# Kernel optimization log

Measured on AMD Instinct MI355X. Metric: run time of the kernel, lower is better.

The kernel has to match this reference:

```python
import jax, jax.numpy as jnp
import numpy as np

E, C, F, K = 8, 768, 3072, 2  # NUM_EXPERTS, EMBED_DIM, FFN_DIM, TOP_K


def setup_inputs() -> dict:
    key = jax.random.key(0)
    k0, k1, k2, k3 = jax.random.split(key, 4)
    B, T = 8, 2048
    return {
        "x": jax.random.normal(k0, (B, T, C), jnp.float32),
        "router_w": jax.random.normal(k1, (E, C), jnp.float32) * 0.02,
        "w1": jax.random.normal(k2, (E, C, F), jnp.float32) * 0.02,
        "b1": jnp.zeros((E, F), jnp.float32),
        "w2": jax.random.normal(k3, (E, F, C), jnp.float32) * 0.02,
        "b2": jnp.zeros((E, C), jnp.float32),
    }


def reference(x, router_w, w1, b1, w2, b2):
    # Dropout is inference-mode identity (eval). GELU is torch's exact (erf) variant.
    B, T, Cc = x.shape
    flat = x.reshape(-1, Cc)                                   # [N, C]
    logits = flat @ router_w.T                                 # [N, E]
    probs = jax.nn.softmax(logits.astype(jnp.float32), axis=-1)
    top_w, top_i = jax.lax.top_k(probs, K)                     # [N, K]
    top_w = (top_w / top_w.sum(-1, keepdims=True)).astype(x.dtype)
    out = jnp.zeros_like(flat)
    for e in range(E):
        # per-token combine weight for expert e (0 if token not routed to e)
        w_e = jnp.sum(top_w * (top_i == e), axis=-1)[:, None]  # [N, 1]
        h = jax.nn.gelu(flat @ w1[e] + b1[e], approximate=False)  # [N, F]
        out = out + w_e * (h @ w2[e] + b2[e])
    return out.reshape(B, T, Cc)
```

## Files before the change

### kernel.cpp

```cpp
#include <hip/hip_runtime.h>
#include <hip/hip_bf16.h>

#define NTOK 16384
#define CDIM 768
#define FDIM 3072
#define NEXP 8
#define NSLOT 32768
#define HBLK 128
#define MAXTILES 263

typedef __attribute__((ext_vector_type(8))) short bf16x8;
typedef __attribute__((ext_vector_type(4))) float f32x4;
typedef __attribute__((ext_vector_type(8))) unsigned short u16x8;

__device__ __forceinline__ unsigned short f2bf(float f) {
  unsigned int u = __float_as_uint(f);
  u += 0x7FFFu + ((u >> 16) & 1u);
  return (unsigned short)(u >> 16);
}
__device__ __forceinline__ float bf2f(unsigned short h) {
  return __uint_as_float((unsigned int)h << 16);
}

__device__ __forceinline__ float fast_gelu(float x) {
  float x2 = x * x;
  float z = x * __builtin_fmaf(0.070565402f, x2, 1.5975981f);
  float s = __builtin_amdgcn_rcpf(1.0f + __expf(-z));
  return x * s;
}

__device__ __forceinline__ void async16(const void* g, void* l) {
  __builtin_amdgcn_global_load_lds(
      (const __attribute__((address_space(1))) unsigned int*)g,
      (__attribute__((address_space(3))) unsigned int*)l, 16, 0, 0);
}

__global__ __launch_bounds__(256)
void k_transpose(const float* __restrict__ src, unsigned short* __restrict__ dst,
                 int R, int Cc)
{
  __shared__ float tle[32][33];
  int e = blockIdx.z;
  int c0 = blockIdx.x * 32, r0 = blockIdx.y * 32;
  int tx = threadIdx.x & 31, ty = threadIdx.x >> 5;
  const float* s = src + (size_t)e * R * Cc;
  unsigned short* d = dst + (size_t)e * R * Cc;
#pragma unroll
  for (int i = 0; i < 4; ++i)
    tle[ty + i * 8][tx] = s[(size_t)(r0 + ty + i * 8) * Cc + c0 + tx];
  __syncthreads();
#pragma unroll
  for (int i = 0; i < 4; ++i)
    d[(size_t)(c0 + ty + i * 8) * R + r0 + tx] = f2bf(tle[tx][ty + i * 8]);
}

__global__ __launch_bounds__(256)
void k_router(const float* __restrict__ x, const float* __restrict__ rw,
              int* __restrict__ tk_e, float* __restrict__ tk_w)
{
  __shared__ float srw[NEXP * CDIM];
  int tid = threadIdx.x;
#pragma unroll
  for (int i = 0; i < (NEXP * CDIM / 4) / 256; ++i)
    ((float4*)srw)[tid + i * 256] = ((const float4*)rw)[tid + i * 256];
  __syncthreads();
  int lane = tid & 63, wid = tid >> 6;
  int t = blockIdx.x * 4 + wid;
  float a[NEXP];
#pragma unroll
  for (int e = 0; e < NEXP; ++e) a[e] = 0.f;
  const float* xr = x + (size_t)t * CDIM;
#pragma unroll
  for (int c = 0; c < CDIM / 64; ++c) {
    float xv = xr[c * 64 + lane];
#pragma unroll
    for (int e = 0; e < NEXP; ++e) a[e] += xv * srw[e * CDIM + c * 64 + lane];
  }
#pragma unroll
  for (int e = 0; e < NEXP; ++e) {
#pragma unroll
    for (int off = 32; off; off >>= 1) a[e] += __shfl_xor(a[e], off);
  }
  if (lane == 0) {
    int i0 = 0; float l0 = a[0];
#pragma unroll
    for (int e = 1; e < NEXP; ++e) if (a[e] > l0) { l0 = a[e]; i0 = e; }
    int i1 = -1; float l1 = -1e30f;
#pragma unroll
    for (int e = 0; e < NEXP; ++e) if (e != i0 && a[e] > l1) { l1 = a[e]; i1 = e; }
    float w0 = 1.f / (1.f + expf(l1 - l0));
    tk_e[2 * t] = i0;     tk_e[2 * t + 1] = i1;
    tk_w[2 * t] = w0;     tk_w[2 * t + 1] = 1.f - w0;
  }
}

__global__ __launch_bounds__(256)
void k_hist(const int* __restrict__ tk_e, int* __restrict__ blockhist)
{
  __shared__ int h[NEXP];
  int tid = threadIdx.x;
  if (tid < NEXP) h[tid] = 0;
  __syncthreads();
  int e = tk_e[blockIdx.x * 256 + tid];
  atomicAdd(&h[e], 1);
  __syncthreads();
  if (tid < NEXP) blockhist[blockIdx.x * NEXP + tid] = h[tid];
}

__global__ __launch_bounds__(512)
void k_scan2(const int* __restrict__ blockhist, int* __restrict__ counts,
             int* __restrict__ offsets, int* __restrict__ tp,
             int* __restrict__ blockbase)
{
  __shared__ int ltot[NEXP];
  __shared__ int loff[NEXP + 1];
  int tid = threadIdx.x;
  int lane = tid & 63, e = tid >> 6;
  int o0 = blockhist[lane * NEXP + e];
  int o1 = blockhist[(64 + lane) * NEXP + e];
  int h0 = o0, h1 = o1;
#pragma unroll
  for (int d = 1; d < 64; d <<= 1) { int v = __shfl_up(h0, d); if (lane >= d) h0 += v; }
  int s0 = __shfl(h0, 63);
#pragma unroll
  for (int d = 1; d < 64; d <<= 1) { int v = __shfl_up(h1, d); if (lane >= d) h1 += v; }
  h1 += s0;
  if (lane == 63) ltot[e] = h1;
  __syncthreads();
  if (tid == 0) {
    loff[0] = 0;
    int tpv = 0; tp[0] = 0;
    for (int k = 0; k < NEXP; ++k) {
      loff[k + 1] = loff[k] + ltot[k];
      counts[k] = ltot[k];
      offsets[k] = loff[k];
      tpv += (ltot[k] + 127) / 128;
      tp[k + 1] = tpv;
    }
    offsets[NEXP] = loff[NEXP];
  }
  __syncthreads();
  int base = loff[e];
  blockbase[lane * NEXP + e]        = base + h0 - o0;
  blockbase[(64 + lane) * NEXP + e] = base + h1 - o1;
}

__global__ __launch_bounds__(256)
void k_assign_gather(const float* __restrict__ x, const int* __restrict__ tk_e,
                     const float* __restrict__ tk_w,
                     const int* __restrict__ blockbase,
                     int* __restrict__ tok2slot, float* __restrict__ slot_w,
                     unsigned short* __restrict__ Xg)
{
  __shared__ int eh[256];
  __shared__ int sslot[256];
  int b = blockIdx.x, tid = threadIdx.x;
  int pick = b * 256 + tid;
  int e = tk_e[pick];
  eh[tid] = e;
  __syncthreads();
  int rank = 0;
  for (int j = 0; j < tid; ++j) rank += (eh[j] == e);
  int slot = blockbase[b * NEXP + e] + rank;
  sslot[tid] = slot;
  tok2slot[pick] = slot;
  slot_w[slot] = tk_w[pick];
  __syncthreads();
  int lane = tid & 63, wid = tid >> 6;
  for (int p = wid * 64; p < wid * 64 + 64; ++p) {
    int token = (b * 256 + p) >> 1;
    int s = sslot[p];
    const float4* src = (const float4*)(x + (size_t)token * CDIM);
    ushort4* dst = (ushort4*)(Xg + (size_t)s * CDIM);
#pragma unroll
    for (int i = 0; i < 3; ++i) {
      float4 v = src[i * 64 + lane];
      ushort4 hh;
      hh.x = f2bf(v.x); hh.y = f2bf(v.y); hh.z = f2bf(v.z); hh.w = f2bf(v.w);
      dst[i * 64 + lane] = hh;
    }
  }
}

__global__ __launch_bounds__(512, 4)
void k_gemm1(const unsigned short* __restrict__ A, int lda,
             const unsigned short* __restrict__ B, int ldb, long sB,
             int Ksteps, const int* __restrict__ counts,
             const int* __restrict__ offsets, const int* __restrict__ tp,
             int t0, const float* __restrict__ bias, int biasStride,
             unsigned short* __restrict__ Hout, int ldh, int gx, int nwg)
{
  __shared__ __align__(16) char lds[3 * 24576];

  int orig = blockIdx.y * gx + blockIdx.x;
  int q = nwg >> 3, r = nwg & 7;
  int xcd = orig & 7, jj = orig >> 3;
  int wgid = (xcd < r ? xcd * (q + 1) : r * (q + 1) + (xcd - r) * q) + jj;
  const int RG = 16;
  int yT = nwg / gx;
  int gsize = gx * RG;
  int rg = wgid / gsize;
  int rem = wgid - rg * gsize;
  int rgs = yT - rg * RG; if (rgs > RG) rgs = RG;
  int bx = rem / rgs;
  int byl = rg * RG + (rem - bx * rgs);
  int by = t0 + byl;

  if (by >= tp[NEXP]) return;
  int e = 0;
  while (by >= tp[e + 1]) ++e;
  int m0 = (by - tp[e]) * 128;
  int cnt = counts[e];
  int rowbase = offsets[e];
  int n0 = bx * 256;

  const unsigned short* Bexp = B + (long)e * sB + (long)n0 * ldb;
  const unsigned short* Aexp = A + (long)(rowbase + m0) * lda;

  int tid = threadIdx.x;
  int lane = tid & 63, wid = tid >> 6;
  int wm = wid >> 2, wn = wid & 3;
  int ar = lane & 15, kg = lane >> 4;
  int kgs = (kg ^ ((ar >> 1) & 3)) << 4;

  int rA0 = tid >> 2;
  int cA0 = tid & 3;
  int ksw = (cA0 ^ ((rA0 >> 1) & 3)) << 3;
  const unsigned short* As0 = Aexp + (long)rA0 * lda + ksw;
  const unsigned short* Bs0 = Bexp + (long)rA0 * ldb + ksw;
  const unsigned short* Bs1 = Bexp + (long)(rA0 + 128) * ldb + ksw;

  f32x4 acc[4][4] = {};

  auto STAGE = [&](int buf, int t) {
    char* bb = lds + buf * 24576;
    int ko = t * 32;
    async16(As0 + ko, bb + wid * 1024);
    async16(Bs0 + ko, bb + 8192 + wid * 1024);
    async16(Bs1 + ko, bb + 16384 + wid * 1024);
  };

  STAGE(0, 0); STAGE(1, 1);
  int cur = 0, nxt2 = 2;

  for (int ks = 0; ks < Ksteps; ++ks) {
    if (ks + 1 < Ksteps) {
      asm volatile("s_waitcnt vmcnt(3)" ::: "memory");
    } else {
      asm volatile("s_waitcnt vmcnt(0)" ::: "memory");
    }
    __builtin_amdgcn_s_barrier();
    asm volatile("" ::: "memory");

    const char* bb = lds + cur * 24576;
    const char* bA = bb + (wm * 64 + ar) * 64 + kgs;
    const char* bB = bb + 8192 + (wn * 64 + ar) * 64 + kgs;
    bf16x8 af[4], bfr[4];
#pragma unroll
    for (int i = 0; i < 4; ++i) af[i] = *(const bf16x8*)(bA + i * 1024);
#pragma unroll
    for (int i = 0; i < 4; ++i) bfr[i] = *(const bf16x8*)(bB + i * 1024);

    if (ks + 2 < Ksteps) STAGE(nxt2, ks + 2);

#pragma unroll
    for (int mi = 0; mi < 4; ++mi)
#pragma unroll
      for (int ni = 0; ni < 4; ++ni)
        acc[mi][ni] = __builtin_amdgcn_mfma_f32_16x16x32_bf16(af[mi], bfr[ni],
                                                              acc[mi][ni], 0, 0, 0);
    cur = (cur == 2) ? 0 : cur + 1;
    nxt2 = (nxt2 == 2) ? 0 : nxt2 + 1;
  }

  unsigned short* st = (unsigned short*)lds;
  __syncthreads();

#pragma unroll
  for (int ni = 0; ni < 4; ++ni) {
    int col = wn * 64 + ni * 16 + ar;
    float bv = bias[e * biasStride + n0 + col];
#pragma unroll
    for (int mi = 0; mi < 4; ++mi) {
#pragma unroll
      for (int rr = 0; rr < 4; ++rr) {
        int row = wm * 64 + mi * 16 + kg * 4 + rr;
        float v = fast_gelu(acc[mi][ni][rr] + bv);
        st[row * 264 + col] = f2bf(v);
      }
    }
  }
  __syncthreads();
  int row = tid >> 2, qq = tid & 3;
  unsigned short* drow = Hout + (long)(byl * 128 + row) * ldh + n0 + qq * 64;
  const unsigned short* srow = st + row * 264 + qq * 64;
#pragma unroll
  for (int i = 0; i < 8; ++i)
    *(u16x8*)(drow + i * 8) = *(const u16x8*)(srow + i * 8);
}

__global__ __launch_bounds__(256, 3)
void k_gemm2(const unsigned short* __restrict__ A, int lda,
             const unsigned short* __restrict__ B, int ldb, long sB,
             int Ksteps, const int* __restrict__ counts,
             const int* __restrict__ offsets, const int* __restrict__ tp,
             int t0, const float* __restrict__ bias, int biasStride,
             unsigned short* __restrict__ Yout, const float* __restrict__ slot_w,
             int gx, int nwg)
{
  __shared__ __align__(16) char lds[3 * 16384];

  int orig = blockIdx.y * gx + blockIdx.x;
  int q = nwg >> 3, r = nwg & 7;
  int xcd = orig & 7, jj = orig >> 3;
  int wgid = (xcd < r ? xcd * (q + 1) : r * (q + 1) + (xcd - r) * q) + jj;
  const int RG = 16;
  int yT = nwg / gx;
  int gsize = gx * RG;
  int rg = wgid / gsize;
  int rem = wgid - rg * gsize;
  int rgs = yT - rg * RG; if (rgs > RG) rgs = RG;
  int bx = rem / rgs;
  int byl = rg * RG + (rem - bx * rgs);
  int by = t0 + byl;

  if (by >= tp[NEXP]) return;
  int e = 0;
  while (by >= tp[e + 1]) ++e;
  int m0 = (by - tp[e]) * 128;
  int cnt = counts[e];
  int rowbase = offsets[e];
  int n0 = bx * 128;

  const unsigned short* Bexp = B + (long)e * sB + (long)n0 * ldb;
  const unsigned short* Aexp = A + (long)(byl * 128) * lda;

  int tid = threadIdx.x;
  int lane = tid & 63, wid = tid >> 6;
  int wm = wid >> 1, wn = wid & 1;
  int ar = lane & 15, kg = lane >> 4;
  int kgs = (kg ^ ((ar >> 1) & 3)) << 4;

  int rA0 = tid >> 2;
  int cA0 = tid & 3;
  int ksw = (cA0 ^ ((rA0 >> 1) & 3)) << 3;
  const unsigned short* As0 = Aexp + (long)rA0 * lda + ksw;
  const unsigned short* As1 = Aexp + (long)(rA0 + 64) * lda + ksw;
  const unsigned short* Bs0 = Bexp + (long)rA0 * ldb + ksw;
  const unsigned short* Bs1 = Bexp + (long)(rA0 + 64) * ldb + ksw;

  f32x4 acc[4][4] = {};

  auto STAGE = [&](int buf, int t) {
    char* bb = lds + buf * 16384;
    int ko = t * 32;
    async16(As0 + ko, bb + wid * 1024);
    async16(As1 + ko, bb + 4096 + wid * 1024);
    async16(Bs0 + ko, bb + 8192 + wid * 1024);
    async16(Bs1 + ko, bb + 12288 + wid * 1024);
  };

  STAGE(0, 0); STAGE(1, 1);
  int cur = 0, nxt2 = 2;

  for (int ks = 0; ks < Ksteps; ++ks) {
    if (ks + 1 < Ksteps) {
      asm volatile("s_waitcnt vmcnt(4)" ::: "memory");
    } else {
      asm volatile("s_waitcnt vmcnt(0)" ::: "memory");
    }
    __builtin_amdgcn_s_barrier();
    asm volatile("" ::: "memory");

    const char* bb = lds + cur * 16384;
    const char* bA = bb + (wm * 64 + ar) * 64 + kgs;
    const char* bB = bb + 8192 + (wn * 64 + ar) * 64 + kgs;
    bf16x8 af[4], bfr[4];
#pragma unroll
    for (int i = 0; i < 4; ++i) af[i] = *(const bf16x8*)(bA + i * 1024);
#pragma unroll
    for (int i = 0; i < 4; ++i) bfr[i] = *(const bf16x8*)(bB + i * 1024);

    if (ks + 2 < Ksteps) STAGE(nxt2, ks + 2);

#pragma unroll
    for (int mi = 0; mi < 4; ++mi)
#pragma unroll
      for (int ni = 0; ni < 4; ++ni)
        acc[mi][ni] = __builtin_amdgcn_mfma_f32_16x16x32_bf16(af[mi], bfr[ni],
                                                              acc[mi][ni], 0, 0, 0);
    cur = (cur == 2) ? 0 : cur + 1;
    nxt2 = (nxt2 == 2) ? 0 : nxt2 + 1;
  }

  unsigned short* st = (unsigned short*)lds;
  __syncthreads();

#pragma unroll
  for (int mi = 0; mi < 4; ++mi) {
#pragma unroll
    for (int rr = 0; rr < 4; ++rr) {
      int rowl = wm * 64 + mi * 16 + kg * 4 + rr;
      float wt = (m0 + rowl < cnt) ? slot_w[rowbase + m0 + rowl] : 0.f;
#pragma unroll
      for (int ni = 0; ni < 4; ++ni) {
        int col = wn * 64 + ni * 16 + ar;
        float v = (acc[mi][ni][rr] + bias[e * biasStride + n0 + col]) * wt;
        st[rowl * 136 + col] = f2bf(v);
      }
    }
  }
  __syncthreads();
  int row = tid >> 1, half = tid & 1;
  if (m0 + row < cnt) {
    unsigned short* drow = Yout + (long)(rowbase + m0 + row) * CDIM + n0 + half * 64;
    const unsigned short* srow = st + row * 136 + half * 64;
#pragma unroll
    for (int i = 0; i < 8; ++i)
      *(u16x8*)(drow + i * 8) = *(const u16x8*)(srow + i * 8);
  }
}

__global__ __launch_bounds__(256)
void k_combine(const unsigned short* __restrict__ Y,
               const int* __restrict__ tok2slot, float* __restrict__ out)
{
  int t = blockIdx.x * 4 + (threadIdx.x >> 6);
  int lane = threadIdx.x & 63;
  int s0 = tok2slot[2 * t], s1 = tok2slot[2 * t + 1];
  const ushort4* y0 = (const ushort4*)(Y + (size_t)s0 * CDIM);
  const ushort4* y1 = (const ushort4*)(Y + (size_t)s1 * CDIM);
  float4* o = (float4*)(out + (size_t)t * CDIM);
#pragma unroll
  for (int i = 0; i < 3; ++i) {
    ushort4 a = y0[i * 64 + lane];
    ushort4 b = y1[i * 64 + lane];
    float4 r;
    r.x = bf2f(a.x) + bf2f(b.x);
    r.y = bf2f(a.y) + bf2f(b.y);
    r.z = bf2f(a.z) + bf2f(b.z);
    r.w = bf2f(a.w) + bf2f(b.w);
    o[i * 64 + lane] = r;
  }
}

extern "C" void kernel_launch(void* const* d_in, const int* in_sizes, int n_in,
                              void* d_out, int out_size, void* d_ws, size_t ws_size,
                              hipStream_t stream) {
  const float* x        = (const float*)d_in[0];
  const float* router_w = (const float*)d_in[1];
  const float* w1       = (const float*)d_in[2];
  const float* b1       = (const float*)d_in[3];
  const float* w2       = (const float*)d_in[4];
  const float* b2       = (const float*)d_in[5];
  float* out = (float*)d_out;

  char* ws = (char*)d_ws;
  size_t off = 0;
  auto alloc = [&](size_t bytes) -> void* {
    void* p = ws + off;
    off = (off + bytes + 255) & ~(size_t)255;
    return p;
  };
  int*   counts     = (int*)alloc(NEXP * 4);
  int*   offsets    = (int*)alloc((NEXP + 1) * 4);
  int*   tp         = (int*)alloc((NEXP + 1) * 4);
  int*   tk_e       = (int*)alloc((size_t)NSLOT * 4);
  float* tk_w       = (float*)alloc((size_t)NSLOT * 4);
  int*   blockhist  = (int*)alloc((size_t)HBLK * NEXP * 4);
  int*   blockbase  = (int*)alloc((size_t)HBLK * NEXP * 4);
  int*   tok2slot   = (int*)alloc((size_t)NSLOT * 4);
  float* slot_w     = (float*)alloc((size_t)NSLOT * 4);
  unsigned short* Yslot = (unsigned short*)alloc((size_t)NSLOT * CDIM * 2);
  unsigned short* w1t = (unsigned short*)alloc((size_t)NEXP * FDIM * CDIM * 2);
  unsigned short* w2t = (unsigned short*)alloc((size_t)NEXP * CDIM * FDIM * 2);
  unsigned short* Xg  = (unsigned short*)alloc((size_t)(NSLOT + 256) * CDIM * 2);
  int TPC = 66;
  if (off + ((size_t)TPC * 128 + 128) * FDIM * 2 > ws_size) TPC = 33;
  unsigned short* H = (unsigned short*)alloc(((size_t)TPC * 128 + 128) * FDIM * 2);

  k_transpose<<<dim3(FDIM / 32, CDIM / 32, NEXP), 256, 0, stream>>>(w1, w1t, CDIM, FDIM);
  k_transpose<<<dim3(CDIM / 32, FDIM / 32, NEXP), 256, 0, stream>>>(w2, w2t, FDIM, CDIM);
  k_router<<<NTOK / 4, 256, 0, stream>>>(x, router_w, tk_e, tk_w);
  k_hist<<<HBLK, 256, 0, stream>>>(tk_e, blockhist);
  k_scan2<<<1, 512, 0, stream>>>(blockhist, counts, offsets, tp, blockbase);
  k_assign_gather<<<HBLK, 256, 0, stream>>>(x, tk_e, tk_w, blockbase,
                                            tok2slot, slot_w, Xg);

  for (int t0 = 0; t0 < MAXTILES; t0 += TPC) {
    int yT = (MAXTILES - t0 < TPC) ? (MAXTILES - t0) : TPC;
    int gx1 = FDIM / 256;
    k_gemm1<<<dim3(gx1, yT), 512, 0, stream>>>(
        Xg, CDIM, w1t, CDIM, (long)FDIM * CDIM, CDIM / 32,
        counts, offsets, tp, t0, b1, FDIM, H, FDIM, gx1, gx1 * yT);
    int gx2 = CDIM / 128;
    k_gemm2<<<dim3(gx2, yT), 256, 0, stream>>>(
        H, FDIM, w2t, FDIM, (long)CDIM * FDIM, FDIM / 32,
        counts, offsets, tp, t0, b2, CDIM, Yslot, slot_w, gx2, gx2 * yT);
  }
  k_combine<<<NTOK / 4, 256, 0, stream>>>(Yslot, tok2slot, out);
}
```

Baseline: 665.6 us.

## Use 256x256 tiles in gemm1 with 8-phase ping-pong LDS pipeline

Expert GEMM1 now computes 256-row by 256-column tiles per workgroup instead of 128x256. It uses 128 KB of double-buffered LDS with K=64 stages, an XOR swizzle, and eight barrier-separated MFMA phases per iteration, with s_setprio raised around the MFMA blocks. Expert tile padding moves to 256 rows and gemm2 is remapped to two 128-row halves per 256-row tile, skipping empty halves. This is meant to raise arithmetic intensity and overlap loads with MFMA. In exchange it cuts occupancy to 2 waves per SIMD, increases padding waste per expert, and adds many barriers.

```diff
diff --git a/kernel.cpp b/kernel.cpp
--- a/kernel.cpp
+++ b/kernel.cpp
@@ -7,7 +7,7 @@
 #define NEXP 8
 #define NSLOT 32768
 #define HBLK 128
-#define MAXTILES 263
+#define MAXT256 135
 
 typedef __attribute__((ext_vector_type(8))) short bf16x8;
 typedef __attribute__((ext_vector_type(4))) float f32x4;
@@ -34,6 +34,10 @@
       (const __attribute__((address_space(1))) unsigned int*)g,
       (__attribute__((address_space(3))) unsigned int*)l, 16, 0, 0);
 }
+
+#define BARRIER() asm volatile("s_barrier" ::: "memory")
+#define LGK0()    asm volatile("s_waitcnt lgkmcnt(0)" ::: "memory")
+#define VMC(n)    asm volatile("s_waitcnt vmcnt(" #n ")" ::: "memory")
 
 __global__ __launch_bounds__(256)
 void k_transpose(const float* __restrict__ src, unsigned short* __restrict__ dst,
@@ -134,7 +138,7 @@
       loff[k + 1] = loff[k] + ltot[k];
       counts[k] = ltot[k];
       offsets[k] = loff[k];
-      tpv += (ltot[k] + 127) / 128;
+      tpv += (ltot[k] + 255) / 256;
       tp[k + 1] = tpv;
     }
     offsets[NEXP] = loff[NEXP];
@@ -182,15 +186,15 @@
   }
 }
 
-__global__ __launch_bounds__(512, 4)
+__global__ __launch_bounds__(512, 2)
 void k_gemm1(const unsigned short* __restrict__ A, int lda,
              const unsigned short* __restrict__ B, int ldb, long sB,
-             int Ksteps, const int* __restrict__ counts,
+             int KI, const int* __restrict__ counts,
              const int* __restrict__ offsets, const int* __restrict__ tp,
              int t0, const float* __restrict__ bias, int biasStride,
              unsigned short* __restrict__ Hout, int ldh, int gx, int nwg)
 {
-  __shared__ __align__(16) char lds[3 * 24576];
+  __shared__ __align__(16) char lds[131072];
 
   int orig = blockIdx.y * gx + blockIdx.x;
   int q = nwg >> 3, r = nwg & 7;
@@ -209,9 +213,8 @@
   if (by >= tp[NEXP]) return;
   int e = 0;
   while (by >= tp[e + 1]) ++e;
-  int m0 = (by - tp[e]) * 128;
-  int cnt = counts[e];
   int rowbase = offsets[e];
+  int m0 = (by - tp[e]) * 256;
   int n0 = bx * 256;
 
   const unsigned short* Bexp = B + (long)e * sB + (long)n0 * ldb;
@@ -221,82 +224,133 @@
   int lane = tid & 63, wid = tid >> 6;
   int wm = wid >> 2, wn = wid & 3;
   int ar = lane & 15, kg = lane >> 4;
-  int kgs = (kg ^ ((ar >> 1) & 3)) << 4;
-
-  int rA0 = tid >> 2;
-  int cA0 = tid & 3;
-  int ksw = (cA0 ^ ((rA0 >> 1) & 3)) << 3;
-  const unsigned short* As0 = Aexp + (long)rA0 * lda + ksw;
-  const unsigned short* Bs0 = Bexp + (long)rA0 * ldb + ksw;
-  const unsigned short* Bs1 = Bexp + (long)(rA0 + 128) * ldb + ksw;
-
-  f32x4 acc[4][4] = {};
-
-  auto STAGE = [&](int buf, int t) {
-    char* bb = lds + buf * 24576;
-    int ko = t * 32;
-    async16(As0 + ko, bb + wid * 1024);
-    async16(Bs0 + ko, bb + 8192 + wid * 1024);
-    async16(Bs1 + ko, bb + 16384 + wid * 1024);
+  int arl = ar & 7;
+
+  const char* pA[2][2];
+  const char* pB[2][2];
+#pragma unroll
+  for (int d = 0; d < 2; ++d)
+#pragma unroll
+    for (int s = 0; s < 2; ++s) {
+      int sw = (((s * 4 + kg) ^ arl) << 4);
+      pA[d][s] = lds + d * 65536 + (wm * 128 + ar) * 128 + sw;
+      pB[d][s] = lds + d * 65536 + 32768 + (wn * 64 + ar) * 128 + sw;
+    }
+
+  int srow = tid >> 3, schunk = tid & 7;
+  int sswz = ((schunk ^ (srow & 7)) << 3);
+  const unsigned short* srcA = Aexp + (long)srow * lda + sswz;
+  const unsigned short* srcB = Bexp + (long)srow * ldb + sswz;
+
+  auto STG_A = [&](int d, int kt, int g) {
+    async16(srcA + (long)g * 64 * lda + kt * 64,
+            lds + d * 65536 + g * 8192 + wid * 1024);
   };
-
-  STAGE(0, 0); STAGE(1, 1);
-  int cur = 0, nxt2 = 2;
-
-  for (int ks = 0; ks < Ksteps; ++ks) {
-    if (ks + 1 < Ksteps) {
-      asm volatile("s_waitcnt vmcnt(3)" ::: "memory");
+  auto STG_B = [&](int d, int kt, int g) {
+    async16(srcB + (long)g * 64 * ldb + kt * 64,
+            lds + d * 65536 + 32768 + g * 8192 + wid * 1024);
+  };
+
+  f32x4 acc[8][4] = {};
+  bf16x8 a[2][4], b[2][4];
+
+#define LDA_(d, h)                                                   \
+  _Pragma("unroll") for (int s = 0; s < 2; ++s)                      \
+  _Pragma("unroll") for (int m = 0; m < 4; ++m)                      \
+    a[s][m] = *(const bf16x8*)(pA[d][s] + (h) * 8192 + m * 2048);
+#define LDB_(d, np)                                                  \
+  _Pragma("unroll") for (int s = 0; s < 2; ++s)                      \
+  _Pragma("unroll") for (int j = 0; j < 2; ++j)                      \
+    b[s][(np) * 2 + j] = *(const bf16x8*)(pB[d][s] + ((np) * 2 + j) * 2048);
+#define MM_(h, np)                                                   \
+  _Pragma("unroll") for (int m = 0; m < 4; ++m)                      \
+  _Pragma("unroll") for (int j = 0; j < 2; ++j) {                    \
+    acc[(h)*4+m][(np)*2+j] = __builtin_amdgcn_mfma_f32_16x16x32_bf16(\
+        a[0][m], b[0][(np)*2+j], acc[(h)*4+m][(np)*2+j], 0, 0, 0);   \
+    acc[(h)*4+m][(np)*2+j] = __builtin_amdgcn_mfma_f32_16x16x32_bf16(\
+        a[1][m], b[1][(np)*2+j], acc[(h)*4+m][(np)*2+j], 0, 0, 0); }
+#define PHTAIL()                                                     \
+  LGK0(); __builtin_amdgcn_sched_barrier(0);                         \
+  __builtin_amdgcn_s_setprio(1)
+#define PHEND()                                                      \
+  __builtin_amdgcn_s_setprio(0); BARRIER()
+
+  STG_A(0, 0, 0); STG_A(0, 0, 1); STG_A(0, 0, 2); STG_A(0, 0, 3);
+  STG_B(0, 0, 0); STG_B(0, 0, 1); STG_B(0, 0, 2); STG_B(0, 0, 3);
+  STG_A(1, 1, 0); STG_A(1, 1, 1);
+  VMC(2);
+  BARRIER();
+
+  for (int i = 0; i < KI; ++i) {
+    int kt1 = 2 * i + 1, kt2 = 2 * i + 2, kt3 = 2 * i + 3;
+    bool cond = (i + 1 < KI);
+    LDA_(0, 0); LDB_(0, 0);
+    STG_A(1, kt1, 2); STG_A(1, kt1, 3);
+    BARRIER(); PHTAIL(); MM_(0, 0); PHEND();
+    LDB_(0, 1);
+    STG_B(1, kt1, 0); STG_B(1, kt1, 1);
+    BARRIER(); PHTAIL(); MM_(0, 1); PHEND();
+    LDA_(0, 1);
+    STG_B(1, kt1, 2); STG_B(1, kt1, 3);
+    BARRIER(); PHTAIL(); MM_(1, 0); PHEND();
+    if (cond) {
+      STG_A(0, kt2, 0); STG_A(0, kt2, 1);
+      VMC(2);
     } else {
-      asm volatile("s_waitcnt vmcnt(0)" ::: "memory");
-    }
-    __builtin_amdgcn_s_barrier();
-    asm volatile("" ::: "memory");
-
-    const char* bb = lds + cur * 24576;
-    const char* bA = bb + (wm * 64 + ar) * 64 + kgs;
-    const char* bB = bb + 8192 + (wn * 64 + ar) * 64 + kgs;
-    bf16x8 af[4], bfr[4];
-#pragma unroll
-    for (int i = 0; i < 4; ++i) af[i] = *(const bf16x8*)(bA + i * 1024);
-#pragma unroll
-    for (int i = 0; i < 4; ++i) bfr[i] = *(const bf16x8*)(bB + i * 1024);
-
-    if (ks + 2 < Ksteps) STAGE(nxt2, ks + 2);
-
-#pragma unroll
-    for (int mi = 0; mi < 4; ++mi)
-#pragma unroll
-      for (int ni = 0; ni < 4; ++ni)
-        acc[mi][ni] = __builtin_amdgcn_mfma_f32_16x16x32_bf16(af[mi], bfr[ni],
-                                                              acc[mi][ni], 0, 0, 0);
-    cur = (cur == 2) ? 0 : cur + 1;
-    nxt2 = (nxt2 == 2) ? 0 : nxt2 + 1;
+      VMC(0);
+    }
+    BARRIER(); PHTAIL(); MM_(1, 1); PHEND();
+    LDA_(1, 0); LDB_(1, 0);
+    if (cond) { STG_A(0, kt2, 2); STG_A(0, kt2, 3); }
+    BARRIER(); PHTAIL(); MM_(0, 0); PHEND();
+    LDB_(1, 1);
+    if (cond) { STG_B(0, kt2, 0); STG_B(0, kt2, 1); }
+    BARRIER(); PHTAIL(); MM_(0, 1); PHEND();
+    LDA_(1, 1);
+    if (cond) { STG_B(0, kt2, 2); STG_B(0, kt2, 3); }
+    BARRIER(); PHTAIL(); MM_(1, 0); PHEND();
+    if (cond) {
+      STG_A(1, kt3, 0); STG_A(1, kt3, 1);
+      VMC(2);
+    }
+    BARRIER(); PHTAIL(); MM_(1, 1); PHEND();
   }
 
   unsigned short* st = (unsigned short*)lds;
   __syncthreads();
-
-#pragma unroll
-  for (int ni = 0; ni < 4; ++ni) {
-    int col = wn * 64 + ni * 16 + ar;
-    float bv = bias[e * biasStride + n0 + col];
-#pragma unroll
-    for (int mi = 0; mi < 4; ++mi) {
-#pragma unroll
-      for (int rr = 0; rr < 4; ++rr) {
-        int row = wm * 64 + mi * 16 + kg * 4 + rr;
-        float v = fast_gelu(acc[mi][ni][rr] + bv);
-        st[row * 264 + col] = f2bf(v);
+#pragma unroll
+  for (int pass = 0; pass < 2; ++pass) {
+    if (wm == pass) {
+#pragma unroll
+      for (int n = 0; n < 4; ++n) {
+        int col = wn * 64 + n * 16 + ar;
+        float bv = bias[e * biasStride + n0 + col];
+#pragma unroll
+        for (int m = 0; m < 8; ++m) {
+#pragma unroll
+          for (int rr = 0; rr < 4; ++rr) {
+            int row = m * 16 + kg * 4 + rr;
+            float v = fast_gelu(acc[m][n][rr] + bv);
+            st[row * 264 + col] = f2bf(v);
+          }
+        }
       }
     }
-  }
-  __syncthreads();
-  int row = tid >> 2, qq = tid & 3;
-  unsigned short* drow = Hout + (long)(byl * 128 + row) * ldh + n0 + qq * 64;
-  const unsigned short* srow = st + row * 264 + qq * 64;
-#pragma unroll
-  for (int i = 0; i < 8; ++i)
-    *(u16x8*)(drow + i * 8) = *(const u16x8*)(srow + i * 8);
+    __syncthreads();
+    int row = tid >> 2, qq = tid & 3;
+    unsigned short* drow =
+        Hout + (long)(byl * 256 + pass * 128 + row) * ldh + n0 + qq * 64;
+    const unsigned short* srow2 = st + row * 264 + qq * 64;
+#pragma unroll
+    for (int i = 0; i < 8; ++i)
+      *(u16x8*)(drow + i * 8) = *(const u16x8*)(srow2 + i * 8);
+    __syncthreads();
+  }
+#undef LDA_
+#undef LDB_
+#undef MM_
+#undef PHTAIL
+#undef PHEND
 }
 
 __global__ __launch_bounds__(256, 3)
@@ -322,18 +376,20 @@
   int rgs = yT - rg * RG; if (rgs > RG) rgs = RG;
   int bx = rem / rgs;
   int byl = rg * RG + (rem - bx * rgs);
-  int by = t0 + byl;
-
+
+  int t256l = byl >> 1, half = byl & 1;
+  int by = t0 + t256l;
   if (by >= tp[NEXP]) return;
   int e = 0;
   while (by >= tp[e + 1]) ++e;
-  int m0 = (by - tp[e]) * 128;
   int cnt = counts[e];
   int rowbase = offsets[e];
+  int m0 = (by - tp[e]) * 256 + half * 128;
+  if (m0 >= cnt) return;
   int n0 = bx * 128;
 
   const unsigned short* Bexp = B + (long)e * sB + (long)n0 * ldb;
-  const unsigned short* Aexp = A + (long)(byl * 128) * lda;
+  const unsigned short* Aexp = A + (long)(t256l * 256 + half * 128) * lda;
 
   int tid = threadIdx.x;
   int lane = tid & 63, wid = tid >> 6;
@@ -411,10 +467,10 @@
     }
   }
   __syncthreads();
-  int row = tid >> 1, half = tid & 1;
+  int row = tid >> 1, hh = tid & 1;
   if (m0 + row < cnt) {
-    unsigned short* drow = Yout + (long)(rowbase + m0 + row) * CDIM + n0 + half * 64;
-    const unsigned short* srow = st + row * 136 + half * 64;
+    unsigned short* drow = Yout + (long)(rowbase + m0 + row) * CDIM + n0 + hh * 64;
+    const unsigned short* srow = st + row * 136 + hh * 64;
 #pragma unroll
     for (int i = 0; i < 8; ++i)
       *(u16x8*)(drow + i * 8) = *(const u16x8*)(srow + i * 8);
@@ -433,14 +489,14 @@
   float4* o = (float4*)(out + (size_t)t * CDIM);
 #pragma unroll
   for (int i = 0; i < 3; ++i) {
-    ushort4 a = y0[i * 64 + lane];
-    ushort4 b = y1[i * 64 + lane];
-    float4 r;
-    r.x = bf2f(a.x) + bf2f(b.x);
-    r.y = bf2f(a.y) + bf2f(b.y);
-    r.z = bf2f(a.z) + bf2f(b.z);
-    r.w = bf2f(a.w) + bf2f(b.w);
-    o[i * 64 + lane] = r;
+    ushort4 aa = y0[i * 64 + lane];
+    ushort4 bb = y1[i * 64 + lane];
+    float4 rr;
+    rr.x = bf2f(aa.x) + bf2f(bb.x);
+    rr.y = bf2f(aa.y) + bf2f(bb.y);
+    rr.z = bf2f(aa.z) + bf2f(bb.z);
+    rr.w = bf2f(aa.w) + bf2f(bb.w);
+    o[i * 64 + lane] = rr;
   }
 }
 
@@ -475,9 +531,9 @@
   unsigned short* w1t = (unsigned short*)alloc((size_t)NEXP * FDIM * CDIM * 2);
   unsigned short* w2t = (unsigned short*)alloc((size_t)NEXP * CDIM * FDIM * 2);
   unsigned short* Xg  = (unsigned short*)alloc((size_t)(NSLOT + 256) * CDIM * 2);
-  int TPC = 66;
-  if (off + ((size_t)TPC * 128 + 128) * FDIM * 2 > ws_size) TPC = 33;
-  unsigned short* H = (unsigned short*)alloc(((size_t)TPC * 128 + 128) * FDIM * 2);
+  int TPC = 42;
+  if (off + (size_t)TPC * 256 * FDIM * 2 > ws_size) TPC = 21;
+  unsigned short* H = (unsigned short*)alloc((size_t)TPC * 256 * FDIM * 2);
 
   k_transpose<<<dim3(FDIM / 32, CDIM / 32, NEXP), 256, 0, stream>>>(w1, w1t, CDIM, FDIM);
   k_transpose<<<dim3(CDIM / 32, FDIM / 32, NEXP), 256, 0, stream>>>(w2, w2t, FDIM, CDIM);
@@ -487,16 +543,16 @@
   k_assign_gather<<<HBLK, 256, 0, stream>>>(x, tk_e, tk_w, blockbase,
                                             tok2slot, slot_w, Xg);
 
-  for (int t0 = 0; t0 < MAXTILES; t0 += TPC) {
-    int yT = (MAXTILES - t0 < TPC) ? (MAXTILES - t0) : TPC;
+  for (int t0 = 0; t0 < MAXT256; t0 += TPC) {
+    int yT = (MAXT256 - t0 < TPC) ? (MAXT256 - t0) : TPC;
     int gx1 = FDIM / 256;
     k_gemm1<<<dim3(gx1, yT), 512, 0, stream>>>(
-        Xg, CDIM, w1t, CDIM, (long)FDIM * CDIM, CDIM / 32,
+        Xg, CDIM, w1t, CDIM, (long)FDIM * CDIM, CDIM / 128,
         counts, offsets, tp, t0, b1, FDIM, H, FDIM, gx1, gx1 * yT);
     int gx2 = CDIM / 128;
-    k_gemm2<<<dim3(gx2, yT), 256, 0, stream>>>(
+    k_gemm2<<<dim3(gx2, 2 * yT), 256, 0, stream>>>(
         H, FDIM, w2t, FDIM, (long)CDIM * FDIM, FDIM / 32,
-        counts, offsets, tp, t0, b2, CDIM, Yslot, slot_w, gx2, gx2 * yT);
+        counts, offsets, tp, t0, b2, CDIM, Yslot, slot_w, gx2, gx2 * 2 * yT);
   }
   k_combine<<<NTOK / 4, 256, 0, stream>>>(Yslot, tok2slot, out);
 }
```

New measurement: 644.3 us. 3.2% less time.
